# Kernel tuning notes

Hardware: AMD Instinct MI355X
Metric: run time of the kernel (lower is better)

## Reference

```python
import jax, jax.numpy as jnp
import numpy as np

B, S, E, H = 2, 2048, 1024, 16
D = E // H  # head_size = 64


def setup_inputs() -> dict:
    key = jax.random.key(0)
    ks = jax.random.split(key, 11)
    sc = 0.02
    return {
        "q": jax.random.normal(ks[0], (B, S, E), jnp.float32),
        "k": jax.random.normal(ks[1], (B, S, E), jnp.float32),
        "v": jax.random.normal(ks[2], (B, S, E), jnp.float32),
        "Wq": jax.random.normal(ks[3], (E, E), jnp.float32) * sc,
        "bq": jnp.zeros((E,), jnp.float32),
        "Wk": jax.random.normal(ks[4], (E, E), jnp.float32) * sc,
        "bk": jnp.zeros((E,), jnp.float32),
        "Wv": jax.random.normal(ks[5], (E, E), jnp.float32) * sc,
        "bv": jnp.zeros((E,), jnp.float32),
        "Wo": jax.random.normal(ks[6], (E, E), jnp.float32) * sc,
        "bo": jnp.zeros((E,), jnp.float32),
    }


def reference(q, k, v, Wq, bq, Wk, bk, Wv, bv, Wo, bo):
    # torch Linear: y = x @ W.T + b
    qh = (q @ Wq.T + bq).reshape(B, S, H, D)
    kh = (k @ Wk.T + bk).reshape(B, S, H, D)
    vh = (v @ Wv.T + bv).reshape(B, S, H, D)
    # NOTE: module scales by 1/sqrt(num_heads), not 1/sqrt(head_size)
    scores = jnp.einsum('bqhe,bkhe->bhqk', qh, kh) / jnp.sqrt(jnp.float32(H))
    attn = jax.nn.softmax(scores, axis=-1)  # dropout is identity in eval
    out = jnp.einsum('bhql,blhd->bqhd', attn, vh)  # [B,S,H,D]
    out = out.reshape(B, S, E)
    return out @ Wo.T + bo
```

## Files before the change

kernel.cpp:

```cpp
#include <hip/hip_runtime.h>

typedef __bf16 bf16x8 __attribute__((ext_vector_type(8)));
typedef __bf16 bf16x4 __attribute__((ext_vector_type(4)));
typedef float  f32x4  __attribute__((ext_vector_type(4)));
typedef short  s16x4  __attribute__((ext_vector_type(4)));

#define AS1 __attribute__((address_space(1)))
#define AS3 __attribute__((address_space(3)))

__device__ inline void gload_lds16(const void* g, void* l) {
  __builtin_amdgcn_global_load_lds((AS1 void*)(g), (AS3 void*)(l), 16, 0, 0);
}

#if __has_builtin(__builtin_amdgcn_exp2f)
#define EXP2(x) __builtin_amdgcn_exp2f(x)
#else
#define EXP2(x) exp2f(x)
#endif

#if __has_builtin(__builtin_amdgcn_mfma_f32_16x16x16bf16_1k)
#define PV_K16 1
#define MFMA16(a, b, c) __builtin_amdgcn_mfma_f32_16x16x16bf16_1k(a, b, c, 0, 0, 0)
#else
#define PV_K16 0
#endif

__device__ inline short bf2s(__bf16 x) {
  union { __bf16 b; short s; } u; u.b = x; return u.s;
}

#define CB 2
#define CS 2048
#define CE 1024
#define CH 16
#define CD 64
#define GM 4096
#define GN 1024
#define GK 1024

#define QSCALE 0.36067376022224087f

#define WS_WQ  0
#define WS_WK  1048576
#define WS_WV  2097152
#define WS_WO  3145728
#define WS_XQ  4194304
#define WS_XK  8388608
#define WS_XV  12582912
#define WS_QH  16777216
#define WS_KH  20971520
#define WS_VT  25165824
#define WS_AO  WS_XQ

__global__ __launch_bounds__(256) void convert_all(
    const float* __restrict__ q, const float* __restrict__ k, const float* __restrict__ v,
    const float* __restrict__ wq, const float* __restrict__ wk,
    const float* __restrict__ wv, const float* __restrict__ wo,
    __bf16* __restrict__ ws) {
  long idx = ((long)blockIdx.x * 256 + threadIdx.x) * 8;
  const float* src;
  __bf16* dst;
  if (idx < 12582912) {
    int a = (int)(idx >> 22);
    long within = idx & 4194303;
    src = (a == 0 ? q : (a == 1 ? k : v)) + within;
    dst = ws + WS_XQ + (long)a * 4194304 + within;
  } else {
    long widx = idx - 12582912;
    int a = (int)(widx >> 20);
    long within = widx & 1048575;
    src = (a == 0 ? wq : (a == 1 ? wk : (a == 2 ? wv : wo))) + within;
    dst = ws + widx;
  }
  float4 f0 = *(const float4*)src;
  float4 f1 = *(const float4*)(src + 4);
  bf16x8 o;
  o[0] = (__bf16)f0.x; o[1] = (__bf16)f0.y; o[2] = (__bf16)f0.z; o[3] = (__bf16)f0.w;
  o[4] = (__bf16)f1.x; o[5] = (__bf16)f1.y; o[6] = (__bf16)f1.z; o[7] = (__bf16)f1.w;
  *(bf16x8*)dst = o;
}

#define GEMM_BK64_BODY(A_PTR, B_PTR, KLEN)                                          \
  __shared__ __bf16 As[8192];                                                       \
  __shared__ __bf16 Bs[8192];                                                       \
  const int tid = threadIdx.x;                                                      \
  const int w = tid >> 6, l = tid & 63;                                             \
  const int wm = w >> 1, wn = w & 1;                                                \
  const int orig = blockIdx.y * gridDim.x + blockIdx.x;                             \
  const int cpx = (gridDim.x * gridDim.y) >> 3;                                     \
  const int wgid = (orig & 7) * cpx + (orig >> 3);                                  \
  const int bm = (wgid / gridDim.x) * 128, bn = (wgid % gridDim.x) * 128;           \
  const int lr = l & 15, lq = l >> 4;                                               \
  f32x4 acc[4][4] = {};                                                             \
  const int srow = w * 8 + (l >> 3);                                                \
  const int scol = ((l & 7) ^ ((l >> 3) & 7)) * 8;                                  \
  const __bf16* ga0 = (A_PTR) + (size_t)(bm + srow) * GK + scol;                    \
  const __bf16* gb0 = (B_PTR) + (size_t)(bn + srow) * GK + scol;                    \
  const int dstg = w * 64 + l;                                                      \
  for (int k0 = 0; k0 < (KLEN); k0 += 64) {                                         \
    __syncthreads();                                                                \
    for (int i = 0; i < 4; i++) {                                                   \
      gload_lds16(ga0 + (size_t)(i * 32) * GK + k0, &As[(i * 256 + dstg) * 8]);     \
      gload_lds16(gb0 + (size_t)(i * 32) * GK + k0, &Bs[(i * 256 + dstg) * 8]);     \
    }                                                                               \
    __syncthreads();                                                                \
    for (int kk = 0; kk < 2; kk++) {                                                \
      bf16x8 af[4], bfr[4];                                                         \
      for (int mi = 0; mi < 4; mi++) {                                              \
        const int row = wm * 64 + mi * 16 + lr;                                     \
        af[mi] = *(const bf16x8*)&As[(row * 8 + ((kk * 4 + lq) ^ (row & 7))) * 8];  \
      }                                                                             \
      for (int ni = 0; ni < 4; ni++) {                                              \
        const int row = wn * 64 + ni * 16 + lr;                                     \
        bfr[ni] = *(const bf16x8*)&Bs[(row * 8 + ((kk * 4 + lq) ^ (row & 7))) * 8]; \
      }                                                                             \
      for (int mi = 0; mi < 4; mi++)                                                \
        for (int ni = 0; ni < 4; ni++)                                              \
          acc[mi][ni] = __builtin_amdgcn_mfma_f32_16x16x32_bf16(af[mi], bfr[ni],    \
                                                                acc[mi][ni], 0, 0, 0); \
    }                                                                               \
  }

__global__ __launch_bounds__(256) void qkv_gemm(
    const __bf16* __restrict__ Xq, const __bf16* __restrict__ Xk, const __bf16* __restrict__ Xv,
    const __bf16* __restrict__ Wq, const __bf16* __restrict__ Wk, const __bf16* __restrict__ Wv,
    const float* __restrict__ bq, const float* __restrict__ bk, const float* __restrict__ bv,
    __bf16* __restrict__ Qh, __bf16* __restrict__ Kh, __bf16* __restrict__ Vt) {
  const int mode = blockIdx.z;
  const __bf16* A  = mode == 0 ? Xq : (mode == 1 ? Xk : Xv);
  const __bf16* Bw = mode == 0 ? Wq : (mode == 1 ? Wk : Wv);
  const float* bias = mode == 0 ? bq : (mode == 1 ? bk : bv);

  GEMM_BK64_BODY(A, Bw, GK)

  const int row0 = bm + wm * 64;
  const int col0 = bn + wn * 64;
  for (int ni = 0; ni < 4; ni++) {
    const int col = col0 + ni * 16 + lr;
    const float bb = bias[col];
    for (int mi = 0; mi < 4; mi++) {
      const int row = row0 + mi * 16 + lq * 4;
      if (mode == 0) {
        for (int r = 0; r < 4; r++)
          Qh[(size_t)(row + r) * GN + col] = (__bf16)((acc[mi][ni][r] + bb) * QSCALE);
      } else if (mode == 1) {
        for (int r = 0; r < 4; r++)
          Kh[(size_t)(row + r) * GN + col] = (__bf16)(acc[mi][ni][r] + bb);
      } else {
        const int b = row >> 11, s = row & 2047;
        const int h = col >> 6, d = col & 63;
        bf16x4 pk;
        for (int r = 0; r < 4; r++) pk[r] = (__bf16)(acc[mi][ni][r] + bb);
        *(bf16x4*)&Vt[(size_t)((b * CH + h) * CD + d) * CS + s] = pk;
      }
    }
  }
}

__global__ __launch_bounds__(256) void gemm_wo(const __bf16* __restrict__ Ain,
                                               const __bf16* __restrict__ Bw,
                                               const float* __restrict__ bias,
                                               float* __restrict__ O) {
  __shared__ __bf16 As[4096];
  __shared__ __bf16 Bs[8192];
  const int tid = threadIdx.x;
  const int w = tid >> 6, l = tid & 63;
  const int orig = blockIdx.y * gridDim.x + blockIdx.x;
  const int cpx = (gridDim.x * gridDim.y) >> 3;
  const int wgid = (orig & 7) * cpx + (orig >> 3);
  const int bm = (wgid / gridDim.x) * 64, bn = (wgid % gridDim.x) * 128;
  const int lr = l & 15, lq = l >> 4;
  f32x4 acc[4][2] = {};
  const int srow = w * 8 + (l >> 3);
  const int scol = ((l & 7) ^ ((l >> 3) & 7)) * 8;
  const __bf16* ga0 = Ain + (size_t)(bm + srow) * GK + scol;
  const __bf16* gb0 = Bw + (size_t)(bn + srow) * GK + scol;
  const int dstg = w * 64 + l;
  for (int k0 = 0; k0 < GK; k0 += 64) {
    __syncthreads();
    for (int i = 0; i < 2; i++)
      gload_lds16(ga0 + (size_t)(i * 32) * GK + k0, &As[(i * 256 + dstg) * 8]);
    for (int i = 0; i < 4; i++)
      gload_lds16(gb0 + (size_t)(i * 32) * GK + k0, &Bs[(i * 256 + dstg) * 8]);
    __syncthreads();
    for (int kk = 0; kk < 2; kk++) {
      bf16x8 af[4], bfr[2];
      for (int mi = 0; mi < 4; mi++) {
        const int row = mi * 16 + lr;
        af[mi] = *(const bf16x8*)&As[(row * 8 + ((kk * 4 + lq) ^ (row & 7))) * 8];
      }
      for (int ni = 0; ni < 2; ni++) {
        const int row = w * 32 + ni * 16 + lr;
        bfr[ni] = *(const bf16x8*)&Bs[(row * 8 + ((kk * 4 + lq) ^ (row & 7))) * 8];
      }
      for (int mi = 0; mi < 4; mi++)
        for (int ni = 0; ni < 2; ni++)
          acc[mi][ni] = __builtin_amdgcn_mfma_f32_16x16x32_bf16(af[mi], bfr[ni],
                                                                acc[mi][ni], 0, 0, 0);
    }
  }

  for (int ni = 0; ni < 2; ni++) {
    const int col = bn + w * 32 + ni * 16 + lr;
    const float bb = bias[col];
    for (int mi = 0; mi < 4; mi++) {
      const int row = bm + mi * 16 + lq * 4;
      for (int r = 0; r < 4; r++)
        O[(size_t)(row + r) * GN + col] = acc[mi][ni][r] + bb;
    }
  }
}

__global__ __launch_bounds__(256, 2) void attn(const __bf16* __restrict__ Qh,
                                               const __bf16* __restrict__ Kh,
                                               const __bf16* __restrict__ Vt,
                                               __bf16* __restrict__ AO) {
  __shared__ __bf16 Ks[8192];
  __shared__ __bf16 Vs[8192];

  const int tid = threadIdx.x, w = tid >> 6, l = tid & 63;
  const int lr = l & 15, lq = l >> 4;
  const int bh = blockIdx.x;
  const int b = bh >> 4, h = bh & 15;
  const int q0 = blockIdx.y * 128 + w * 32;

  bf16x8 qf[2][2];
  for (int mi = 0; mi < 2; mi++)
    for (int kk = 0; kk < 2; kk++)
      qf[mi][kk] = *(const bf16x8*)&Qh[((size_t)b * CS + q0 + mi * 16 + lr) * CE + h * CD + kk * 32 + lq * 8];

  f32x4 o[2][4] = {};
  float lsum[2] = {0.f, 0.f};
#if !PV_K16
  const bool hi_half = (lq & 1);
#endif

  for (int kt = 0; kt < CS / 128; kt++) {
    __syncthreads();
    for (int i = 0; i < 4; i++) {
      const int j = w * 2 + (i >> 1), hf = i & 1;
      const int key = (hf * 64 + l) ^ ((j & 3) * 2);
      gload_lds16(&Kh[((size_t)b * CS + kt * 128 + key) * CE + h * CD + j * 8],
                  &Ks[(j * 128 + hf * 64) * 8]);
    }
    for (int i = 0; i < 4; i++) {
      const int j2 = w * 4 + i;
      const int d = l ^ ((j2 & 1) * 4);
      gload_lds16(&Vt[((size_t)bh * CD + d) * CS + kt * 128 + j2 * 8],
                  &Vs[(j2 * 64) * 8]);
    }
    __syncthreads();

    f32x4 sa[2][8] = {};
    for (int kk = 0; kk < 2; kk++) {
      bf16x8 kf[8];
      for (int ni = 0; ni < 8; ni++)
        kf[ni] = *(const bf16x8*)&Ks[((kk * 4 + lq) * 128 + ((ni * 16 + lr) ^ (lq * 2))) * 8];
      for (int mi = 0; mi < 2; mi++)
        for (int ni = 0; ni < 8; ni++)
          sa[mi][ni] = __builtin_amdgcn_mfma_f32_16x16x32_bf16(kf[ni], qf[mi][kk], sa[mi][ni], 0, 0, 0);
    }

#if PV_K16
    for (int ni = 0; ni < 8; ni++) {
      s16x4 pa4[2];
      for (int mi = 0; mi < 2; mi++)
        for (int r = 0; r < 4; r++) {
          const float p = EXP2(sa[mi][ni][r]);
          lsum[mi] += p;
          pa4[mi][r] = bf2s((__bf16)p);
        }
      const int j2 = ni * 2 + (lq >> 1);
      const int base = j2 * 64;
      const int sw = (j2 & 1) * 4;
      for (int di = 0; di < 4; di++) {
        const int dslot = (di * 16 + lr) ^ sw;
        const s16x4 vb4 = *(const s16x4*)&Vs[(base + dslot) * 8 + (lq & 1) * 4];
        for (int mi = 0; mi < 2; mi++)
          o[mi][di] = MFMA16(pa4[mi], vb4, o[mi][di]);
      }
    }
#else
    for (int ni = 0; ni < 8; ni++) {
      bf16x8 pa[2];
      for (int mi = 0; mi < 2; mi++) {
        bf16x8 f;
        for (int r = 0; r < 4; r++) {
          const float p = EXP2(sa[mi][ni][r]);
          lsum[mi] += p;
          const __bf16 bv2 = (__bf16)p;
          f[r]     = hi_half ? (__bf16)0.f : bv2;
          f[4 + r] = hi_half ? bv2 : (__bf16)0.f;
        }
        pa[mi] = f;
      }
      for (int di = 0; di < 4; di++) {
        const bf16x8 vbf = *(const bf16x8*)&Vs[((ni * 2 + (lq >> 1)) * 64 + ((di * 16 + lr) ^ ((lq >> 1) * 4))) * 8];
        for (int mi = 0; mi < 2; mi++)
          o[mi][di] = __builtin_amdgcn_mfma_f32_16x16x32_bf16(pa[mi], vbf, o[mi][di], 0, 0, 0);
      }
    }
#endif
  }

  for (int mi = 0; mi < 2; mi++) {
    lsum[mi] += __shfl_xor(lsum[mi], 16, 64);
    lsum[mi] += __shfl_xor(lsum[mi], 32, 64);
  }

  for (int mi = 0; mi < 2; mi++) {
    f32x4 rv;
    for (int r = 0; r < 4; r++) rv[r] = 1.0f / __shfl(lsum[mi], lq * 4 + r, 64);
    for (int di = 0; di < 4; di++)
      for (int r = 0; r < 4; r++) {
        const size_t s = q0 + mi * 16 + lq * 4 + r;
        AO[((size_t)b * CS + s) * CE + h * CD + di * 16 + lr] = (__bf16)(o[mi][di][r] * rv[r]);
      }
  }
}

extern "C" void kernel_launch(void* const* d_in, const int* in_sizes, int n_in,
                              void* d_out, int out_size, void* d_ws, size_t ws_size,
                              hipStream_t stream) {
  (void)in_sizes; (void)n_in; (void)out_size; (void)ws_size;
  const float* q  = (const float*)d_in[0];
  const float* k  = (const float*)d_in[1];
  const float* v  = (const float*)d_in[2];
  const float* Wq = (const float*)d_in[3];
  const float* bq = (const float*)d_in[4];
  const float* Wk = (const float*)d_in[5];
  const float* bk = (const float*)d_in[6];
  const float* Wv = (const float*)d_in[7];
  const float* bv = (const float*)d_in[8];
  const float* Wo = (const float*)d_in[9];
  const float* bo = (const float*)d_in[10];

  __bf16* ws = (__bf16*)d_ws;
  __bf16 *Wq_b = ws + WS_WQ, *Wk_b = ws + WS_WK, *Wv_b = ws + WS_WV, *Wo_b = ws + WS_WO;
  __bf16 *Xq = ws + WS_XQ, *Xk = ws + WS_XK, *Xv = ws + WS_XV;
  __bf16 *Qh = ws + WS_QH, *Kh = ws + WS_KH, *Vt = ws + WS_VT;
  __bf16 *AO = ws + WS_AO;

  convert_all<<<8192, 256, 0, stream>>>(q, k, v, Wq, Wk, Wv, Wo, ws);

  qkv_gemm<<<dim3(GN / 128, GM / 128, 3), 256, 0, stream>>>(
      Xq, Xk, Xv, Wq_b, Wk_b, Wv_b, bq, bk, bv, Qh, Kh, Vt);

  attn<<<dim3(CB * CH, CS / 128), 256, 0, stream>>>(Qh, Kh, Vt, AO);

  gemm_wo<<<dim3(GN / 128, GM / 64), 256, 0, stream>>>(AO, Wo_b, bo, (float*)d_out);
}
```

Measured before the change: 221.6 us.

## Shrink QKV GEMM tiles to 64x128 and loop over Q/K/V modes per block

The QKV projection kernel moves from 128x128 tiles, with one grid z-slice per projection, to 64x128 tiles where each block handles its tile for all three projections in sequence. The grid becomes 8x64 = 512 blocks instead of 8x32x3 = 768, and each wave computes a 64x32 subtile. This lowers LDS use and accumulator registers per block, which may raise occupancy, and keeps the same weight columns hot across modes. In exchange each block does three times the serial work, and the smaller tiles reuse each loaded A and B element less.

```diff
diff --git a/kernel.cpp b/kernel.cpp
--- a/kernel.cpp
+++ b/kernel.cpp
@@ -80,78 +80,74 @@
   *(bf16x8*)dst = o;
 }
 
-#define GEMM_BK64_BODY(A_PTR, B_PTR, KLEN)                                          \
-  __shared__ __bf16 As[8192];                                                       \
-  __shared__ __bf16 Bs[8192];                                                       \
-  const int tid = threadIdx.x;                                                      \
-  const int w = tid >> 6, l = tid & 63;                                             \
-  const int wm = w >> 1, wn = w & 1;                                                \
-  const int orig = blockIdx.y * gridDim.x + blockIdx.x;                             \
-  const int cpx = (gridDim.x * gridDim.y) >> 3;                                     \
-  const int wgid = (orig & 7) * cpx + (orig >> 3);                                  \
-  const int bm = (wgid / gridDim.x) * 128, bn = (wgid % gridDim.x) * 128;           \
-  const int lr = l & 15, lq = l >> 4;                                               \
-  f32x4 acc[4][4] = {};                                                             \
-  const int srow = w * 8 + (l >> 3);                                                \
-  const int scol = ((l & 7) ^ ((l >> 3) & 7)) * 8;                                  \
-  const __bf16* ga0 = (A_PTR) + (size_t)(bm + srow) * GK + scol;                    \
-  const __bf16* gb0 = (B_PTR) + (size_t)(bn + srow) * GK + scol;                    \
-  const int dstg = w * 64 + l;                                                      \
-  for (int k0 = 0; k0 < (KLEN); k0 += 64) {                                         \
-    __syncthreads();                                                                \
-    for (int i = 0; i < 4; i++) {                                                   \
-      gload_lds16(ga0 + (size_t)(i * 32) * GK + k0, &As[(i * 256 + dstg) * 8]);     \
-      gload_lds16(gb0 + (size_t)(i * 32) * GK + k0, &Bs[(i * 256 + dstg) * 8]);     \
-    }                                                                               \
-    __syncthreads();                                                                \
-    for (int kk = 0; kk < 2; kk++) {                                                \
-      bf16x8 af[4], bfr[4];                                                         \
-      for (int mi = 0; mi < 4; mi++) {                                              \
-        const int row = wm * 64 + mi * 16 + lr;                                     \
-        af[mi] = *(const bf16x8*)&As[(row * 8 + ((kk * 4 + lq) ^ (row & 7))) * 8];  \
-      }                                                                             \
-      for (int ni = 0; ni < 4; ni++) {                                              \
-        const int row = wn * 64 + ni * 16 + lr;                                     \
-        bfr[ni] = *(const bf16x8*)&Bs[(row * 8 + ((kk * 4 + lq) ^ (row & 7))) * 8]; \
-      }                                                                             \
-      for (int mi = 0; mi < 4; mi++)                                                \
-        for (int ni = 0; ni < 4; ni++)                                              \
-          acc[mi][ni] = __builtin_amdgcn_mfma_f32_16x16x32_bf16(af[mi], bfr[ni],    \
-                                                                acc[mi][ni], 0, 0, 0); \
-    }                                                                               \
-  }
-
 __global__ __launch_bounds__(256) void qkv_gemm(
     const __bf16* __restrict__ Xq, const __bf16* __restrict__ Xk, const __bf16* __restrict__ Xv,
     const __bf16* __restrict__ Wq, const __bf16* __restrict__ Wk, const __bf16* __restrict__ Wv,
     const float* __restrict__ bq, const float* __restrict__ bk, const float* __restrict__ bv,
     __bf16* __restrict__ Qh, __bf16* __restrict__ Kh, __bf16* __restrict__ Vt) {
-  const int mode = blockIdx.z;
-  const __bf16* A  = mode == 0 ? Xq : (mode == 1 ? Xk : Xv);
-  const __bf16* Bw = mode == 0 ? Wq : (mode == 1 ? Wk : Wv);
-  const float* bias = mode == 0 ? bq : (mode == 1 ? bk : bv);
-
-  GEMM_BK64_BODY(A, Bw, GK)
-
-  const int row0 = bm + wm * 64;
-  const int col0 = bn + wn * 64;
-  for (int ni = 0; ni < 4; ni++) {
-    const int col = col0 + ni * 16 + lr;
-    const float bb = bias[col];
-    for (int mi = 0; mi < 4; mi++) {
-      const int row = row0 + mi * 16 + lq * 4;
-      if (mode == 0) {
-        for (int r = 0; r < 4; r++)
-          Qh[(size_t)(row + r) * GN + col] = (__bf16)((acc[mi][ni][r] + bb) * QSCALE);
-      } else if (mode == 1) {
-        for (int r = 0; r < 4; r++)
-          Kh[(size_t)(row + r) * GN + col] = (__bf16)(acc[mi][ni][r] + bb);
-      } else {
-        const int b = row >> 11, s = row & 2047;
-        const int h = col >> 6, d = col & 63;
-        bf16x4 pk;
-        for (int r = 0; r < 4; r++) pk[r] = (__bf16)(acc[mi][ni][r] + bb);
-        *(bf16x4*)&Vt[(size_t)((b * CH + h) * CD + d) * CS + s] = pk;
+  __shared__ __bf16 As[4096];
+  __shared__ __bf16 Bs[8192];
+  const int tid = threadIdx.x;
+  const int w = tid >> 6, l = tid & 63;
+  const int orig = blockIdx.y * gridDim.x + blockIdx.x;
+  const int cpx = (gridDim.x * gridDim.y) >> 3;
+  const int wgid = (orig & 7) * cpx + (orig >> 3);
+  const int bm = (wgid / gridDim.x) * 64, bn = (wgid % gridDim.x) * 128;
+  const int lr = l & 15, lq = l >> 4;
+  const int srow = w * 8 + (l >> 3);
+  const int scol = ((l & 7) ^ ((l >> 3) & 7)) * 8;
+  const int dstg = w * 64 + l;
+
+  for (int mode = 0; mode < 3; mode++) {
+    const __bf16* A  = mode == 0 ? Xq : (mode == 1 ? Xk : Xv);
+    const __bf16* Bw = mode == 0 ? Wq : (mode == 1 ? Wk : Wv);
+    const float* bias = mode == 0 ? bq : (mode == 1 ? bk : bv);
+    const __bf16* ga0 = A  + (size_t)(bm + srow) * GK + scol;
+    const __bf16* gb0 = Bw + (size_t)(bn + srow) * GK + scol;
+
+    f32x4 acc[4][2] = {};
+    for (int k0 = 0; k0 < GK; k0 += 64) {
+      __syncthreads();
+      for (int i = 0; i < 2; i++)
+        gload_lds16(ga0 + (size_t)(i * 32) * GK + k0, &As[(i * 256 + dstg) * 8]);
+      for (int i = 0; i < 4; i++)
+        gload_lds16(gb0 + (size_t)(i * 32) * GK + k0, &Bs[(i * 256 + dstg) * 8]);
+      __syncthreads();
+      for (int kk = 0; kk < 2; kk++) {
+        bf16x8 af[4], bfr[2];
+        for (int mi = 0; mi < 4; mi++) {
+          const int row = mi * 16 + lr;
+          af[mi] = *(const bf16x8*)&As[(row * 8 + ((kk * 4 + lq) ^ (row & 7))) * 8];
+        }
+        for (int ni = 0; ni < 2; ni++) {
+          const int row = w * 32 + ni * 16 + lr;
+          bfr[ni] = *(const bf16x8*)&Bs[(row * 8 + ((kk * 4 + lq) ^ (row & 7))) * 8];
+        }
+        for (int mi = 0; mi < 4; mi++)
+          for (int ni = 0; ni < 2; ni++)
+            acc[mi][ni] = __builtin_amdgcn_mfma_f32_16x16x32_bf16(af[mi], bfr[ni],
+                                                                  acc[mi][ni], 0, 0, 0);
+      }
+    }
+
+    for (int ni = 0; ni < 2; ni++) {
+      const int col = bn + w * 32 + ni * 16 + lr;
+      const float bb = bias[col];
+      for (int mi = 0; mi < 4; mi++) {
+        const int row = bm + mi * 16 + lq * 4;
+        if (mode == 0) {
+          for (int r = 0; r < 4; r++)
+            Qh[(size_t)(row + r) * GN + col] = (__bf16)((acc[mi][ni][r] + bb) * QSCALE);
+        } else if (mode == 1) {
+          for (int r = 0; r < 4; r++)
+            Kh[(size_t)(row + r) * GN + col] = (__bf16)(acc[mi][ni][r] + bb);
+        } else {
+          const int b = row >> 11, s = row & 2047;
+          const int h = col >> 6, d = col & 63;
+          bf16x4 pk;
+          for (int r = 0; r < 4; r++) pk[r] = (__bf16)(acc[mi][ni][r] + bb);
+          *(bf16x4*)&Vt[(size_t)((b * CH + h) * CD + d) * CS + s] = pk;
+        }
       }
     }
   }
@@ -343,7 +339,7 @@
 
   convert_all<<<8192, 256, 0, stream>>>(q, k, v, Wq, Wk, Wv, Wo, ws);
 
-  qkv_gemm<<<dim3(GN / 128, GM / 128, 3), 256, 0, stream>>>(
+  qkv_gemm<<<dim3(8, 64), 256, 0, stream>>>(
       Xq, Xk, Xv, Wq_b, Wk_b, Wv_b, bq, bk, bv, Qh, Kh, Vt);
 
   attn<<<dim3(CB * CH, CS / 128), 256, 0, stream>>>(Qh, Kh, Vt, AO);
```

Measured after the change: 223.7 us. Within noise of the previous version (+0.9%).
